# Performance work log

Measured on AMD Instinct MI355X. Metric: run time of the kernel, lower is better.

## Reference

```python
import jax, jax.numpy as jnp
import numpy as np

D_MODEL = 1024
NUM_HEADS = 16
HEAD_DIM = D_MODEL // NUM_HEADS
EPS = 1e-06


def setup_inputs() -> dict:
    key = jax.random.key(0)
    ks = jax.random.split(key, 7)
    B, T, D = 4, 4096, D_MODEL
    scale = 1.0 / np.sqrt(D)
    x = jax.random.normal(ks[0], (B, T, D), dtype=jnp.float32)
    Wq = jax.random.normal(ks[1], (D, D), dtype=jnp.float32) * scale
    Wk = jax.random.normal(ks[2], (D, D), dtype=jnp.float32) * scale
    Wv = jax.random.normal(ks[3], (D, D), dtype=jnp.float32) * scale
    Wo = jax.random.normal(ks[4], (D, D), dtype=jnp.float32) * scale
    Wg = jax.random.normal(ks[5], (D, D), dtype=jnp.float32) * scale
    bg = jnp.zeros((D,), dtype=jnp.float32)
    return {"x": x, "Wq": Wq, "Wk": Wk, "Wv": Wv, "Wo": Wo, "Wg": Wg, "bg": bg}


def phi(x):
    return jax.nn.elu(x) + 1.0


def reference(x, Wq, Wk, Wv, Wo, Wg, bg):
    B, T, D = x.shape
    H, Hd = NUM_HEADS, HEAD_DIM
    # torch nn.Linear: y = x @ W.T
    q = phi((x @ Wq.T).reshape(B, T, H, Hd))
    k = phi((x @ Wk.T).reshape(B, T, H, Hd))
    v = (x @ Wv.T).reshape(B, T, H, Hd)
    k_sum = k.sum(axis=1)                              # [B,H,Hd]
    kv_sum = jnp.einsum('bthd,bthd->bhd', k, v)        # [B,H,Hd] (elementwise-product reduction, as in source)
    # out[b,t,h,v] = sum_d q[b,t,h,d]*kv_sum[b,h,d], identical for every v
    s = jnp.einsum('bthd,bhd->bth', q, kv_sum)         # [B,T,H]
    z = jnp.einsum('bthd,bhd->bth', q, k_sum) + EPS    # [B,T,H]
    out = (s / z)[..., None] * jnp.ones((Hd,), dtype=x.dtype)  # broadcast over head_dim
    out = out.reshape(B, T, D)
    gate = jax.nn.sigmoid(x @ Wg.T + bg)
    return gate * out + (1.0 - gate) * x
```

## Files before the change

kernel.cpp:

```cpp
#include <hip/hip_runtime.h>

#define D_MODEL 1024
#define TSEQ    4096
#define BATCH   4
#define MROWS   (BATCH * TSEQ)
#define KDIM    1024
#define NDIM    1024
#define EPSV    1e-6f

typedef __attribute__((ext_vector_type(8))) short short8;
typedef __attribute__((ext_vector_type(4))) float floatx4;

__device__ inline unsigned short f2bf(float f) {
  unsigned u = __float_as_uint(f);
  unsigned r = (u + 0x7FFFu + ((u >> 16) & 1u)) >> 16;
  return (unsigned short)r;
}
__device__ inline float phi_f(float x) { return x > 0.f ? x + 1.f : __expf(x); }

#define GLD16(gp, lp) __builtin_amdgcn_global_load_lds( \
    (const __attribute__((address_space(1))) void*)(gp), \
    (__attribute__((address_space(3))) void*)(lp), 16, 0, 0)

#define VMCNT8() asm volatile("s_waitcnt vmcnt(8)" ::: "memory")
#define VMCNT0() asm volatile("s_waitcnt vmcnt(0)" ::: "memory")

#define NX4 4194304
#define NW4 262144
#define NZ4 2048

__global__ __launch_bounds__(256) void prep_kernel(
    const float* __restrict__ x,  const float* __restrict__ wq,
    const float* __restrict__ wk, const float* __restrict__ wv,
    const float* __restrict__ wg,
    unsigned short* __restrict__ xb,  unsigned short* __restrict__ wqb,
    unsigned short* __restrict__ wkb, unsigned short* __restrict__ wvb,
    unsigned short* __restrict__ wgb, float* __restrict__ zbase)
{
  long i = (long)blockIdx.x * 256 + threadIdx.x;
  const float* src; unsigned short* dst; long j = i;
  if (j < NX4) { src = x; dst = xb; }
  else {
    j -= NX4;
    if (j < NW4) { src = wq; dst = wqb; }
    else { j -= NW4;
      if (j < NW4) { src = wk; dst = wkb; }
      else { j -= NW4;
        if (j < NW4) { src = wv; dst = wvb; }
        else { j -= NW4;
          if (j < NW4) { src = wg; dst = wgb; }
          else { j -= NW4;
            if (j < NZ4) { float4 zz = {0.f,0.f,0.f,0.f}; ((float4*)zbase)[j] = zz; }
            return;
          }
        }
      }
    }
  }
  float4 f = ((const float4*)src)[j];
  ushort4 o;
  o.x = f2bf(f.x); o.y = f2bf(f.y); o.z = f2bf(f.z); o.w = f2bf(f.w);
  ((ushort4*)dst)[j] = o;
}

#define BM 256
#define BN 128
#define BK 64
#define NSTEP (KDIM / BK)

__global__ __launch_bounds__(512, 1) void gemm_kv_kernel(
    const unsigned short* __restrict__ A,
    const unsigned short* __restrict__ Wk, const unsigned short* __restrict__ Wv,
    float* __restrict__ ksum, float* __restrict__ kvsum)
{
  __shared__ __align__(16) unsigned short As0[BM * BK], As1[BM * BK];
  __shared__ __align__(16) unsigned short Bk0[BN * BK], Bk1[BN * BK];
  __shared__ __align__(16) unsigned short Bv0[BN * BK], Bv1[BN * BK];

  const int bid = blockIdx.x;
  const int sw  = (bid & 7) * 64 + (bid >> 3);
  const int bn  = sw & 7;
  const int bm  = sw >> 3;

  const int tid  = threadIdx.x;
  const int lane = tid & 63;
  const int w    = tid >> 6;
  const int wr   = (w >> 2) * 128;
  const int wc   = (w & 3) * 32;
  const int la   = lane & 15;
  const int l4   = lane >> 4;

  floatx4 ak[8][2], av[8][2];
#pragma unroll
  for (int i = 0; i < 8; i++)
#pragma unroll
    for (int j = 0; j < 2; j++) {
      floatx4 zz = {0.f,0.f,0.f,0.f}; ak[i][j] = zz; av[i][j] = zz;
    }

  const unsigned short* Ablk = A  + (size_t)bm * BM * KDIM;
  const unsigned short* Bkb  = Wk + (size_t)bn * BN * KDIM;
  const unsigned short* Bvb  = Wv + (size_t)bn * BN * KDIM;

  int aoff[4], boff[2];
#pragma unroll
  for (int i = 0; i < 4; i++) {
    int s = tid + i * 512; int r = s >> 3;
    aoff[i] = r * KDIM + (((s & 7) ^ (r & 7)) << 3);
  }
#pragma unroll
  for (int i = 0; i < 2; i++) {
    int s = tid + i * 512; int r = s >> 3;
    boff[i] = r * KDIM + (((s & 7) ^ (r & 7)) << 3);
  }

  auto stage8 = [&](unsigned short* Aw, unsigned short* Bkw, unsigned short* Bvw,
                    int kt) {
#pragma unroll
    for (int i = 0; i < 4; ++i)
      GLD16(Ablk + aoff[i] + kt, Aw + (size_t)(tid + i * 512) * 8);
#pragma unroll
    for (int i = 0; i < 2; ++i) {
      GLD16(Bkb + boff[i] + kt, Bkw + (size_t)(tid + i * 512) * 8);
      GLD16(Bvb + boff[i] + kt, Bvw + (size_t)(tid + i * 512) * 8);
    }
  };

  const int sl0 = (0 * 4 + l4) ^ (la & 7);
  const int sl1 = (1 * 4 + l4) ^ (la & 7);

  auto kphases = [&](const unsigned short* Ar, const unsigned short* Bkr,
                     const unsigned short* Bvr) {
    short8 bkf[2][2], bvf[2][2];
#pragma unroll
    for (int p = 0; p < 4; ++p) {
      short8 af[2][2];
#pragma unroll
      for (int rp = 0; rp < 2; ++rp) {
        int row = wr + (2 * p + rp) * 16 + la;
        af[rp][0] = *(const short8*)(Ar + row * BK + sl0 * 8);
        af[rp][1] = *(const short8*)(Ar + row * BK + sl1 * 8);
      }
      if (p == 0) {
#pragma unroll
        for (int j = 0; j < 2; ++j) {
          int row = wc + j * 16 + la;
          bkf[j][0] = *(const short8*)(Bkr + row * BK + sl0 * 8);
          bkf[j][1] = *(const short8*)(Bkr + row * BK + sl1 * 8);
          bvf[j][0] = *(const short8*)(Bvr + row * BK + sl0 * 8);
          bvf[j][1] = *(const short8*)(Bvr + row * BK + sl1 * 8);
        }
      }
      __builtin_amdgcn_s_barrier();
      __builtin_amdgcn_s_setprio(1);
#pragma unroll
      for (int rp = 0; rp < 2; ++rp)
#pragma unroll
        for (int j = 0; j < 2; ++j)
#pragma unroll
          for (int kk = 0; kk < 2; ++kk) {
            ak[2*p+rp][j] = __builtin_amdgcn_mfma_f32_16x16x32_bf16(
                af[rp][kk], bkf[j][kk], ak[2*p+rp][j], 0, 0, 0);
            av[2*p+rp][j] = __builtin_amdgcn_mfma_f32_16x16x32_bf16(
                af[rp][kk], bvf[j][kk], av[2*p+rp][j], 0, 0, 0);
          }
      __builtin_amdgcn_s_setprio(0);
      __builtin_amdgcn_s_barrier();
    }
  };

  stage8(As0, Bk0, Bv0, 0);
  stage8(As1, Bk1, Bv1, BK);
  VMCNT8();
  __builtin_amdgcn_s_barrier();

  for (int st2 = 0; st2 < NSTEP; st2 += 2) {
    kphases(As0, Bk0, Bv0);
    if (st2 + 2 < NSTEP) { stage8(As0, Bk0, Bv0, (st2 + 2) * BK); VMCNT8(); }
    else                 { VMCNT0(); }
    __builtin_amdgcn_s_barrier();
    kphases(As1, Bk1, Bv1);
    if (st2 + 3 < NSTEP) {
      stage8(As1, Bk1, Bv1, (st2 + 3) * BK); VMCNT8();
      __builtin_amdgcn_s_barrier();
    } else if (st2 + 2 < NSTEP) {
      VMCNT0();
      __builtin_amdgcn_s_barrier();
    }
  }

  const int b = bm >> 4;
  float kp[2] = {0.f, 0.f};
  float vp[2] = {0.f, 0.f};
#pragma unroll
  for (int j = 0; j < 2; j++)
#pragma unroll
    for (int mi = 0; mi < 8; mi++)
#pragma unroll
      for (int r = 0; r < 4; r++) {
        float kk = phi_f(ak[mi][j][r]);
        kp[j] += kk;
        vp[j] += kk * av[mi][j][r];
      }
#pragma unroll
  for (int j = 0; j < 2; j++) {
    kp[j] += __shfl_xor(kp[j], 16, 64); kp[j] += __shfl_xor(kp[j], 32, 64);
    vp[j] += __shfl_xor(vp[j], 16, 64); vp[j] += __shfl_xor(vp[j], 32, 64);
  }
  if (lane < 16) {
#pragma unroll
    for (int j = 0; j < 2; j++) {
      int col = bn * BN + wc + j * 16 + lane;
      atomicAdd(ksum  + (size_t)b * D_MODEL + col, kp[j]);
      atomicAdd(kvsum + (size_t)b * D_MODEL + col, vp[j]);
    }
  }
}

__global__ __launch_bounds__(512, 1) void gemm_qg_kernel(
    const unsigned short* __restrict__ A,
    const unsigned short* __restrict__ Wq, const unsigned short* __restrict__ Wg,
    const float* __restrict__ x, const float* __restrict__ bg,
    const float* __restrict__ ksum, const float* __restrict__ kvsum,
    float* __restrict__ out)
{
  __shared__ __align__(16) unsigned short As0[BM * BK], As1[BM * BK];
  __shared__ __align__(16) unsigned short Bq0[BN * BK], Bq1[BN * BK];
  __shared__ __align__(16) unsigned short Bg0[BN * BK], Bg1[BN * BK];
  __shared__ float o_lds[2 * BM];

  const int bid = blockIdx.x;
  const int sw  = (bid & 7) * 64 + (bid >> 3);
  const int bn  = sw & 7;
  const int bm  = sw >> 3;

  const int tid  = threadIdx.x;
  const int lane = tid & 63;
  const int w    = tid >> 6;
  const int is_g = w >> 2;
  const int wl   = w & 3;
  const int wr   = (wl >> 1) * 128;
  const int wc   = (wl & 1) * 64;
  const int la   = lane & 15;
  const int l4   = lane >> 4;

  floatx4 acc[8][4];
#pragma unroll
  for (int i = 0; i < 8; i++)
#pragma unroll
    for (int j = 0; j < 4; j++) { floatx4 zz = {0.f,0.f,0.f,0.f}; acc[i][j] = zz; }

  const unsigned short* Ablk = A  + (size_t)bm * BM * KDIM;
  const unsigned short* Bqb  = Wq + (size_t)bn * BN * KDIM;
  const unsigned short* Bgb  = Wg + (size_t)bn * BN * KDIM;

  int aoff[4], boff[2];
#pragma unroll
  for (int i = 0; i < 4; i++) {
    int s = tid + i * 512; int r = s >> 3;
    aoff[i] = r * KDIM + (((s & 7) ^ (r & 7)) << 3);
  }
#pragma unroll
  for (int i = 0; i < 2; i++) {
    int s = tid + i * 512; int r = s >> 3;
    boff[i] = r * KDIM + (((s & 7) ^ (r & 7)) << 3);
  }

  auto stage8 = [&](unsigned short* Aw, unsigned short* Bqw, unsigned short* Bgw,
                    int kt) {
#pragma unroll
    for (int i = 0; i < 4; ++i)
      GLD16(Ablk + aoff[i] + kt, Aw + (size_t)(tid + i * 512) * 8);
#pragma unroll
    for (int i = 0; i < 2; ++i) {
      GLD16(Bqb + boff[i] + kt, Bqw + (size_t)(tid + i * 512) * 8);
      GLD16(Bgb + boff[i] + kt, Bgw + (size_t)(tid + i * 512) * 8);
    }
  };

  const int sl0 = (0 * 4 + l4) ^ (la & 7);
  const int sl1 = (1 * 4 + l4) ^ (la & 7);

  auto kphases = [&](const unsigned short* Ar, const unsigned short* Br) {
    short8 bf[4][2];
#pragma unroll
    for (int p = 0; p < 4; ++p) {
      short8 af[2][2];
#pragma unroll
      for (int rp = 0; rp < 2; ++rp) {
        int row = wr + (2 * p + rp) * 16 + la;
        af[rp][0] = *(const short8*)(Ar + row * BK + sl0 * 8);
        af[rp][1] = *(const short8*)(Ar + row * BK + sl1 * 8);
      }
      if (p == 0) {
#pragma unroll
        for (int j = 0; j < 4; ++j) {
          int row = wc + j * 16 + la;
          bf[j][0] = *(const short8*)(Br + row * BK + sl0 * 8);
          bf[j][1] = *(const short8*)(Br + row * BK + sl1 * 8);
        }
      }
      __builtin_amdgcn_s_barrier();
      __builtin_amdgcn_s_setprio(1);
#pragma unroll
      for (int rp = 0; rp < 2; ++rp)
#pragma unroll
        for (int j = 0; j < 4; ++j)
#pragma unroll
          for (int kk = 0; kk < 2; ++kk)
            acc[2*p+rp][j] = __builtin_amdgcn_mfma_f32_16x16x32_bf16(
                af[rp][kk], bf[j][kk], acc[2*p+rp][j], 0, 0, 0);
      __builtin_amdgcn_s_setprio(0);
      __builtin_amdgcn_s_barrier();
    }
  };

  stage8(As0, Bq0, Bg0, 0);
  stage8(As1, Bq1, Bg1, BK);
  VMCNT8();
  __builtin_amdgcn_s_barrier();

  for (int st2 = 0; st2 < NSTEP; st2 += 2) {
    kphases(As0, is_g ? Bg0 : Bq0);
    if (st2 + 2 < NSTEP) { stage8(As0, Bq0, Bg0, (st2 + 2) * BK); VMCNT8(); }
    else                 { VMCNT0(); }
    __builtin_amdgcn_s_barrier();
    kphases(As1, is_g ? Bg1 : Bq1);
    if (st2 + 3 < NSTEP) {
      stage8(As1, Bq1, Bg1, (st2 + 3) * BK); VMCNT8();
      __builtin_amdgcn_s_barrier();
    } else if (st2 + 2 < NSTEP) {
      VMCNT0();
      __builtin_amdgcn_s_barrier();
    }
  }

  const int b  = bm >> 4;
  const int ro = l4 * 4;
  const int co = la;
  const int hl = wc >> 6;

  if (!is_g) {
    float kvv[4], ksv[4];
#pragma unroll
    for (int j = 0; j < 4; j++) {
      int col = bn * BN + wc + j * 16 + co;
      kvv[j] = kvsum[(size_t)b * D_MODEL + col];
      ksv[j] = ksum [(size_t)b * D_MODEL + col];
    }
#pragma unroll
    for (int mi = 0; mi < 8; mi++)
#pragma unroll
      for (int r = 0; r < 4; r++) {
        float s = 0.f, z = 0.f;
#pragma unroll
        for (int j = 0; j < 4; j++) {
          float qq = phi_f(acc[mi][j][r]);
          s += qq * kvv[j]; z += qq * ksv[j];
        }
#pragma unroll
        for (int m = 1; m < 16; m <<= 1) {
          s += __shfl_xor(s, m, 64);
          z += __shfl_xor(z, m, 64);
        }
        if (co == 0) o_lds[hl * BM + wr + mi * 16 + ro + r] = s / (z + EPSV);
      }
  }
  __syncthreads();
  if (is_g) {
    float bgv[4];
#pragma unroll
    for (int j = 0; j < 4; j++) bgv[j] = bg[bn * BN + wc + j * 16 + co];
#pragma unroll
    for (int mi = 0; mi < 8; mi++)
#pragma unroll
      for (int r = 0; r < 4; r++) {
        int rowl = wr + mi * 16 + ro + r;
        int grow = bm * BM + rowl;
        float ov = o_lds[hl * BM + rowl];
#pragma unroll
        for (int j = 0; j < 4; j++) {
          int gcol = bn * BN + wc + j * 16 + co;
          float gt = 1.f / (1.f + __expf(-(acc[mi][j][r] + bgv[j])));
          float xv = x[(size_t)grow * D_MODEL + gcol];
          out[(size_t)grow * D_MODEL + gcol] = gt * ov + (1.f - gt) * xv;
        }
      }
  }
}

extern "C" void kernel_launch(void* const* d_in, const int* in_sizes, int n_in,
                              void* d_out, int out_size, void* d_ws, size_t ws_size,
                              hipStream_t stream) {
  (void)in_sizes; (void)n_in; (void)out_size; (void)ws_size;
  const float* x  = (const float*)d_in[0];
  const float* Wq = (const float*)d_in[1];
  const float* Wk = (const float*)d_in[2];
  const float* Wv = (const float*)d_in[3];
  const float* Wg = (const float*)d_in[5];
  const float* bg = (const float*)d_in[6];
  float* out = (float*)d_out;

  char* ws = (char*)d_ws;
  const size_t xel = (size_t)MROWS * D_MODEL;
  const size_t wel = (size_t)NDIM * KDIM;
  unsigned short* xbf = (unsigned short*)ws; ws += xel * 2;
  unsigned short* wqb = (unsigned short*)ws; ws += wel * 2;
  unsigned short* wkb = (unsigned short*)ws; ws += wel * 2;
  unsigned short* wvb = (unsigned short*)ws; ws += wel * 2;
  unsigned short* wgb = (unsigned short*)ws; ws += wel * 2;
  float* ksum  = (float*)ws; ws += (size_t)BATCH * D_MODEL * 4;
  float* kvsum = (float*)ws; ws += (size_t)BATCH * D_MODEL * 4;

  const long total4 = (long)NX4 + 4L * NW4 + NZ4;
  prep_kernel<<<(int)((total4 + 255) / 256), 256, 0, stream>>>(
      x, Wq, Wk, Wv, Wg, xbf, wqb, wkb, wvb, wgb, ksum);

  gemm_kv_kernel<<<512, 512, 0, stream>>>(xbf, wkb, wvb, ksum, kvsum);

  gemm_qg_kernel<<<512, 512, 0, stream>>>(xbf, wqb, wgb, x, bg, ksum, kvsum, out);
}
```

Measured before the change: 298.6 us.

## Interleave global-to-LDS prefetch loads across MFMA phases in both GEMM kernels

Replaces the bulk stage-then-wait prefetch with loads spread across the four compute phases of each k-step. The A tile is split into 32-row quarters so each phase issues part of the next tiles' loads. The last quarter of the next buffer is issued at the start of the following step, and the wait moves to the end of phase 3 with a vmcnt(7) threshold. The aim is to spread memory traffic over the compute so MFMA issue is not stalled by clustered loads or a late wait, at the cost of subtle vmcnt accounting and ordering risks.

```diff
diff --git a/kernel.cpp b/kernel.cpp
--- a/kernel.cpp
+++ b/kernel.cpp
@@ -22,7 +22,7 @@
     (const __attribute__((address_space(1))) void*)(gp), \
     (__attribute__((address_space(3))) void*)(lp), 16, 0, 0)
 
-#define VMCNT8() asm volatile("s_waitcnt vmcnt(8)" ::: "memory")
+#define VMCNT7() asm volatile("s_waitcnt vmcnt(7)" ::: "memory")
 #define VMCNT0() asm volatile("s_waitcnt vmcnt(0)" ::: "memory")
 
 #define NX4 4194304
@@ -102,35 +102,35 @@
   const unsigned short* Bkb  = Wk + (size_t)bn * BN * KDIM;
   const unsigned short* Bvb  = Wv + (size_t)bn * BN * KDIM;
 
-  int aoff[4], boff[2];
-#pragma unroll
-  for (int i = 0; i < 4; i++) {
-    int s = tid + i * 512; int r = s >> 3;
-    aoff[i] = r * KDIM + (((s & 7) ^ (r & 7)) << 3);
-  }
+  const int lr  = tid >> 3;
+  const int slt = tid & 7;
+  const int arb = (lr & 31) + ((lr >> 5) << 7);
+  const int aG  = arb * KDIM + ((slt ^ (lr & 7)) << 3);
+  const int aL  = arb * BK + slt * 8;
+  int boff[2], bL[2];
 #pragma unroll
   for (int i = 0; i < 2; i++) {
     int s = tid + i * 512; int r = s >> 3;
     boff[i] = r * KDIM + (((s & 7) ^ (r & 7)) << 3);
-  }
-
-  auto stage8 = [&](unsigned short* Aw, unsigned short* Bkw, unsigned short* Bvw,
-                    int kt) {
-#pragma unroll
-    for (int i = 0; i < 4; ++i)
-      GLD16(Ablk + aoff[i] + kt, Aw + (size_t)(tid + i * 512) * 8);
-#pragma unroll
-    for (int i = 0; i < 2; ++i) {
-      GLD16(Bkb + boff[i] + kt, Bkw + (size_t)(tid + i * 512) * 8);
-      GLD16(Bvb + boff[i] + kt, Bvw + (size_t)(tid + i * 512) * 8);
-    }
+    bL[i]   = s * 8;
+  }
+
+  auto SA = [&](unsigned short* dst, int s, int p) {
+    GLD16(Ablk + aG + (32 * p) * KDIM + s * BK, dst + aL + p * (32 * BK));
+  };
+  auto SB = [&](const unsigned short* g, unsigned short* dst, int s, int i) {
+    GLD16(g + boff[i] + s * BK, dst + bL[i]);
   };
 
   const int sl0 = (0 * 4 + l4) ^ (la & 7);
   const int sl1 = (1 * 4 + l4) ^ (la & 7);
 
-  auto kphases = [&](const unsigned short* Ar, const unsigned short* Bkr,
-                     const unsigned short* Bvr) {
+  auto kstep = [&](const unsigned short* Ar, const unsigned short* Bkr,
+                   const unsigned short* Bvr, unsigned short* AwStr,
+                   unsigned short* Aw, unsigned short* Bkw, unsigned short* Bvw,
+                   int t) {
+    const bool s1 = (t + 1 < NSTEP);
+    const bool s2 = (t + 2 < NSTEP);
     short8 bkf[2][2], bvf[2][2];
 #pragma unroll
     for (int p = 0; p < 4; ++p) {
@@ -150,7 +150,12 @@
           bvf[j][0] = *(const short8*)(Bvr + row * BK + sl0 * 8);
           bvf[j][1] = *(const short8*)(Bvr + row * BK + sl1 * 8);
         }
-      }
+        if (s1) SA(AwStr, t + 1, 3);
+      }
+      if (p == 1 && s2) { SA(Aw, t + 2, 0); SB(Bkb, Bkw, t + 2, 0); }
+      if (p == 2 && s2) { SA(Aw, t + 2, 1); SB(Bkb, Bkw, t + 2, 1);
+                          SB(Bvb, Bvw, t + 2, 0); }
+      if (p == 3 && s2) { SA(Aw, t + 2, 2); SB(Bvb, Bvw, t + 2, 1); }
       __builtin_amdgcn_s_barrier();
       __builtin_amdgcn_s_setprio(1);
 #pragma unroll
@@ -165,28 +170,27 @@
                 af[rp][kk], bvf[j][kk], av[2*p+rp][j], 0, 0, 0);
           }
       __builtin_amdgcn_s_setprio(0);
+      if (p == 3 && s1) {
+        if (t + 1 == NSTEP - 1) VMCNT0(); else VMCNT7();
+      }
       __builtin_amdgcn_s_barrier();
     }
   };
 
-  stage8(As0, Bk0, Bv0, 0);
-  stage8(As1, Bk1, Bv1, BK);
-  VMCNT8();
+#pragma unroll
+  for (int p = 0; p < 4; ++p) SA(As0, 0, p);
+  SB(Bkb, Bk0, 0, 0); SB(Bkb, Bk0, 0, 1);
+  SB(Bvb, Bv0, 0, 0); SB(Bvb, Bv0, 0, 1);
+#pragma unroll
+  for (int p = 0; p < 3; ++p) SA(As1, 1, p);
+  SB(Bkb, Bk1, 1, 0); SB(Bkb, Bk1, 1, 1);
+  SB(Bvb, Bv1, 1, 0); SB(Bvb, Bv1, 1, 1);
+  VMCNT7();
   __builtin_amdgcn_s_barrier();
 
-  for (int st2 = 0; st2 < NSTEP; st2 += 2) {
-    kphases(As0, Bk0, Bv0);
-    if (st2 + 2 < NSTEP) { stage8(As0, Bk0, Bv0, (st2 + 2) * BK); VMCNT8(); }
-    else                 { VMCNT0(); }
-    __builtin_amdgcn_s_barrier();
-    kphases(As1, Bk1, Bv1);
-    if (st2 + 3 < NSTEP) {
-      stage8(As1, Bk1, Bv1, (st2 + 3) * BK); VMCNT8();
-      __builtin_amdgcn_s_barrier();
-    } else if (st2 + 2 < NSTEP) {
-      VMCNT0();
-      __builtin_amdgcn_s_barrier();
-    }
+  for (int t = 0; t < NSTEP; t += 2) {
+    kstep(As0, Bk0, Bv0, As1, As0, Bk0, Bv0, t);
+    kstep(As1, Bk1, Bv1, As0, As1, Bk1, Bv1, t + 1);
   }
 
   const int b = bm >> 4;
@@ -254,34 +258,36 @@
   const unsigned short* Bqb  = Wq + (size_t)bn * BN * KDIM;
   const unsigned short* Bgb  = Wg + (size_t)bn * BN * KDIM;
 
-  int aoff[4], boff[2];
-#pragma unroll
-  for (int i = 0; i < 4; i++) {
-    int s = tid + i * 512; int r = s >> 3;
-    aoff[i] = r * KDIM + (((s & 7) ^ (r & 7)) << 3);
-  }
+  const int lr  = tid >> 3;
+  const int slt = tid & 7;
+  const int arb = (lr & 31) + ((lr >> 5) << 7);
+  const int aG  = arb * KDIM + ((slt ^ (lr & 7)) << 3);
+  const int aL  = arb * BK + slt * 8;
+  int boff[2], bL[2];
 #pragma unroll
   for (int i = 0; i < 2; i++) {
     int s = tid + i * 512; int r = s >> 3;
     boff[i] = r * KDIM + (((s & 7) ^ (r & 7)) << 3);
-  }
-
-  auto stage8 = [&](unsigned short* Aw, unsigned short* Bqw, unsigned short* Bgw,
-                    int kt) {
-#pragma unroll
-    for (int i = 0; i < 4; ++i)
-      GLD16(Ablk + aoff[i] + kt, Aw + (size_t)(tid + i * 512) * 8);
-#pragma unroll
-    for (int i = 0; i < 2; ++i) {
-      GLD16(Bqb + boff[i] + kt, Bqw + (size_t)(tid + i * 512) * 8);
-      GLD16(Bgb + boff[i] + kt, Bgw + (size_t)(tid + i * 512) * 8);
-    }
+    bL[i]   = s * 8;
+  }
+
+  auto SA = [&](unsigned short* dst, int s, int p) {
+    GLD16(Ablk + aG + (32 * p) * KDIM + s * BK, dst + aL + p * (32 * BK));
+  };
+  auto SB = [&](const unsigned short* g, unsigned short* dst, int s, int i) {
+    GLD16(g + boff[i] + s * BK, dst + bL[i]);
   };
 
   const int sl0 = (0 * 4 + l4) ^ (la & 7);
   const int sl1 = (1 * 4 + l4) ^ (la & 7);
 
-  auto kphases = [&](const unsigned short* Ar, const unsigned short* Br) {
+  auto kstep = [&](const unsigned short* Ar, const unsigned short* Bqr,
+                   const unsigned short* Bgr, unsigned short* AwStr,
+                   unsigned short* Aw, unsigned short* Bqw, unsigned short* Bgw,
+                   int t) {
+    const bool s1 = (t + 1 < NSTEP);
+    const bool s2 = (t + 2 < NSTEP);
+    const unsigned short* Br = is_g ? Bgr : Bqr;
     short8 bf[4][2];
 #pragma unroll
     for (int p = 0; p < 4; ++p) {
@@ -299,7 +305,12 @@
           bf[j][0] = *(const short8*)(Br + row * BK + sl0 * 8);
           bf[j][1] = *(const short8*)(Br + row * BK + sl1 * 8);
         }
-      }
+        if (s1) SA(AwStr, t + 1, 3);
+      }
+      if (p == 1 && s2) { SA(Aw, t + 2, 0); SB(Bqb, Bqw, t + 2, 0); }
+      if (p == 2 && s2) { SA(Aw, t + 2, 1); SB(Bqb, Bqw, t + 2, 1);
+                          SB(Bgb, Bgw, t + 2, 0); }
+      if (p == 3 && s2) { SA(Aw, t + 2, 2); SB(Bgb, Bgw, t + 2, 1); }
       __builtin_amdgcn_s_barrier();
       __builtin_amdgcn_s_setprio(1);
 #pragma unroll
@@ -311,28 +322,27 @@
             acc[2*p+rp][j] = __builtin_amdgcn_mfma_f32_16x16x32_bf16(
                 af[rp][kk], bf[j][kk], acc[2*p+rp][j], 0, 0, 0);
       __builtin_amdgcn_s_setprio(0);
+      if (p == 3 && s1) {
+        if (t + 1 == NSTEP - 1) VMCNT0(); else VMCNT7();
+      }
       __builtin_amdgcn_s_barrier();
     }
   };
 
-  stage8(As0, Bq0, Bg0, 0);
-  stage8(As1, Bq1, Bg1, BK);
-  VMCNT8();
+#pragma unroll
+  for (int p = 0; p < 4; ++p) SA(As0, 0, p);
+  SB(Bqb, Bq0, 0, 0); SB(Bqb, Bq0, 0, 1);
+  SB(Bgb, Bg0, 0, 0); SB(Bgb, Bg0, 0, 1);
+#pragma unroll
+  for (int p = 0; p < 3; ++p) SA(As1, 1, p);
+  SB(Bqb, Bq1, 1, 0); SB(Bqb, Bq1, 1, 1);
+  SB(Bgb, Bg1, 1, 0); SB(Bgb, Bg1, 1, 1);
+  VMCNT7();
   __builtin_amdgcn_s_barrier();
 
-  for (int st2 = 0; st2 < NSTEP; st2 += 2) {
-    kphases(As0, is_g ? Bg0 : Bq0);
-    if (st2 + 2 < NSTEP) { stage8(As0, Bq0, Bg0, (st2 + 2) * BK); VMCNT8(); }
-    else                 { VMCNT0(); }
-    __builtin_amdgcn_s_barrier();
-    kphases(As1, is_g ? Bg1 : Bq1);
-    if (st2 + 3 < NSTEP) {
-      stage8(As1, Bq1, Bg1, (st2 + 3) * BK); VMCNT8();
-      __builtin_amdgcn_s_barrier();
-    } else if (st2 + 2 < NSTEP) {
-      VMCNT0();
-      __builtin_amdgcn_s_barrier();
-    }
+  for (int t = 0; t < NSTEP; t += 2) {
+    kstep(As0, Bq0, Bg0, As1, As0, Bq0, Bg0, t);
+    kstep(As1, Bq1, Bg1, As0, As1, Bq1, Bg1, t + 1);
   }
 
   const int b  = bm >> 4;
```

New measurement: 286.2 us. 1.04x faster.
